# Kernel optimization log

Hardware: AMD Instinct MI355X
Metric: run time of the kernel (lower is better)

## Reference

```python
import jax, jax.numpy as jnp
import numpy as np

EMBED_DIM = 1024
NUM_HEADS = 16
HEAD_DIM = EMBED_DIM // NUM_HEADS
R_QKV = 256
R_OUT = 256
B, T = 4, 2048


def setup_inputs() -> dict:
    key = jax.random.key(0)
    k1, k2, k3, k4, k5 = jax.random.split(key, 5)
    s = 0.02
    return {
        "x": jax.random.normal(k1, (B, T, EMBED_DIM), dtype=jnp.float32),
        "W_qkv_v": jax.random.normal(k2, (R_QKV, EMBED_DIM), dtype=jnp.float32) * s,
        "W_qkv_u": jax.random.normal(k3, (3 * EMBED_DIM, R_QKV), dtype=jnp.float32) * s,
        "W_o_v": jax.random.normal(k4, (R_OUT, EMBED_DIM), dtype=jnp.float32) * s,
        "W_o_u": jax.random.normal(k5, (EMBED_DIM, R_OUT), dtype=jnp.float32) * s,
    }


def reference(x, W_qkv_v, W_qkv_u, W_o_v, W_o_u):
    Bq, Tq, C = x.shape
    H, D = NUM_HEADS, HEAD_DIM
    # low-rank qkv projection: x @ V^T @ U^T (torch Linear weight is [out,in])
    qkv = (x @ W_qkv_v.T) @ W_qkv_u.T  # [B,T,3C]
    q, k, v = jnp.split(qkv, 3, axis=-1)
    # split heads -> [B,H,T,D]
    q = q.reshape(Bq, Tq, H, D).transpose(0, 2, 1, 3)
    k = k.reshape(Bq, Tq, H, D).transpose(0, 2, 1, 3)
    v = v.reshape(Bq, Tq, H, D).transpose(0, 2, 1, 3)
    scale = 1.0 / jnp.sqrt(jnp.asarray(D, dtype=x.dtype))
    scores = jnp.einsum('bhtd,bhsd->bhts', q, k) * scale  # [B,H,T,T]
    # softmax in fp32 then cast back, matching torch.softmax(dtype=float32)
    attn = jax.nn.softmax(scores.astype(jnp.float32), axis=-1).astype(q.dtype)
    y = jnp.einsum('bhts,bhsd->bhtd', attn, v)  # [B,H,T,D]
    y = y.transpose(0, 2, 1, 3).reshape(Bq, Tq, C)  # merge heads
    # low-rank output projection
    y = (y @ W_o_v.T) @ W_o_u.T
    return y
```

## Files before the change

### kernel.cpp

```cpp
#include <hip/hip_runtime.h>
#include <hip/hip_bf16.h>

typedef __attribute__((ext_vector_type(8))) short short8;
typedef __attribute__((ext_vector_type(4))) float f32x4;
typedef __attribute__((ext_vector_type(16))) float f32x16;
typedef unsigned short u16;
typedef unsigned int u32;

__device__ __forceinline__ void gload_lds16(const void* g, void* l) {
  typedef const __attribute__((address_space(1))) u32 gu32;
  typedef __attribute__((address_space(3))) u32 lu32;
  __builtin_amdgcn_global_load_lds((gu32*)g, (lu32*)l, 16, 0, 0);
}

__device__ __forceinline__ u16 f2bf(float f) {
  union { float f; u32 u; } v; v.f = f;
  u32 u = v.u + 0x7FFFu + ((v.u >> 16) & 1u);
  return (u16)(u >> 16);
}

__device__ __forceinline__ u32 cvtpk(float lo, float hiv) {
  u32 r;
  asm("v_cvt_pk_bf16_f32 %0, %1, %2" : "=v"(r) : "v"(lo), "v"(hiv));
  return r;
}

__device__ __forceinline__ void plswap(u32& a, u32& b) {
  asm("v_permlane32_swap_b32 %0, %1" : "+v"(a), "+v"(b));
}

__device__ __forceinline__ float fexp2(float x) {
  float r;
  asm("v_exp_f32 %0, %1" : "=v"(r) : "v"(x));
  return r;
}

__device__ __forceinline__ short8 lds_read8(const u16* base, int byteoff) {
  return *(const short8*)((const char*)base + byteoff);
}

__global__ __launch_bounds__(256) void cast_w_kernel(
    const float* __restrict__ wv, const float* __restrict__ wu,
    const float* __restrict__ wov, const float* __restrict__ wou,
    u16* __restrict__ dst) {
  const long N0 = 262144, N1 = N0 + 786432, N2 = N1 + 262144, N3 = N2 + 262144;
  long i = (long)(blockIdx.x * 256 + threadIdx.x) * 8;
  if (i >= N3) return;
  const float* s;
  if (i < N0) s = wv + i;
  else if (i < N1) s = wu + (i - N0);
  else if (i < N2) s = wov + (i - N1);
  else s = wou + (i - N2);
  float4 a = *(const float4*)s;
  float4 b = *(const float4*)(s + 4);
  short8 o;
  o[0] = (short)f2bf(a.x); o[1] = (short)f2bf(a.y);
  o[2] = (short)f2bf(a.z); o[3] = (short)f2bf(a.w);
  o[4] = (short)f2bf(b.x); o[5] = (short)f2bf(b.y);
  o[6] = (short)f2bf(b.z); o[7] = (short)f2bf(b.w);
  *(short8*)(dst + i) = o;
}

template<int BM, int BN, int MR, int NR, typename OutT>
__global__ __launch_bounds__(256) void gemm_bt(
    OutT* __restrict__ C, const u16* __restrict__ A, const u16* __restrict__ B,
    int N, int K) {
  __shared__ u16 As[BM * 64];
  __shared__ u16 Bs[BN * 64];
  const int tid = threadIdx.x;
  const int l = tid & 63, w = tid >> 6;
  const int wr = w >> 1, wc = w & 1;
  const int bm = blockIdx.x * BM, bn = blockIdx.y * BN;
  const int srow = l >> 3, sslot = (l & 7) ^ srow;

  f32x4 acc[MR][NR] = {};

  const u16* Ag = A + (long)(bm + srow) * K + sslot * 8;
  const u16* Bg = B + (long)(bn + srow) * K + sslot * 8;
  constexpr int CA = BM / 32, CB = BN / 32;

  for (int kt = 0; kt < K; kt += 64) {
#pragma unroll
    for (int c = 0; c < CA; ++c) {
      int ch = w * CA + c;
      gload_lds16(Ag + (long)ch * 8 * K + kt, (char*)As + ch * 1024);
    }
#pragma unroll
    for (int c = 0; c < CB; ++c) {
      int ch = w * CB + c;
      gload_lds16(Bg + (long)ch * 8 * K + kt, (char*)Bs + ch * 1024);
    }
    __syncthreads();
    short8 af[MR][2], bf[NR][2];
#pragma unroll
    for (int i = 0; i < MR; ++i)
#pragma unroll
      for (int kk = 0; kk < 2; ++kk) {
        int row = wr * (MR * 16) + i * 16 + (l & 15);
        af[i][kk] = lds_read8(As, row * 128 + (((kk * 4 + (l >> 4)) ^ (l & 7)) * 16));
      }
#pragma unroll
    for (int j = 0; j < NR; ++j)
#pragma unroll
      for (int kk = 0; kk < 2; ++kk) {
        int col = wc * (NR * 16) + j * 16 + (l & 15);
        bf[j][kk] = lds_read8(Bs, col * 128 + (((kk * 4 + (l >> 4)) ^ (l & 7)) * 16));
      }
#pragma unroll
    for (int kk = 0; kk < 2; ++kk)
#pragma unroll
      for (int i = 0; i < MR; ++i)
#pragma unroll
        for (int j = 0; j < NR; ++j)
          acc[i][j] = __builtin_amdgcn_mfma_f32_16x16x32_bf16(
              af[i][kk], bf[j][kk], acc[i][j], 0, 0, 0);
    __syncthreads();
  }
#pragma unroll
  for (int i = 0; i < MR; ++i)
#pragma unroll
    for (int j = 0; j < NR; ++j) {
      int row = bm + wr * (MR * 16) + i * 16 + (l >> 4) * 4;
      int col = bn + wc * (NR * 16) + j * 16 + (l & 15);
#pragma unroll
      for (int r = 0; r < 4; ++r) {
        if constexpr (sizeof(OutT) == 4) {
          C[(long)(row + r) * N + col] = acc[i][j][r];
        } else {
          ((u16*)C)[(long)(row + r) * N + col] = f2bf(acc[i][j][r]);
        }
      }
    }
}

__global__ __launch_bounds__(256) void gemm_a32(
    u16* __restrict__ C, const float* __restrict__ A, const u16* __restrict__ B,
    int N, int K) {
  constexpr int BM = 64, BN = 64, MR = 2, NR = 2;
  __shared__ u16 As[BM * 64];
  __shared__ u16 Bs[BN * 64];
  const int tid = threadIdx.x;
  const int l = tid & 63, w = tid >> 6;
  const int wr = w >> 1, wc = w & 1;
  const int bm = blockIdx.x * BM, bn = blockIdx.y * BN;
  const int srow = l >> 3, sslot = (l & 7) ^ srow;

  f32x4 acc[MR][NR] = {};
  const u16* Bg = B + (long)(bn + srow) * K + sslot * 8;

  for (int kt = 0; kt < K; kt += 64) {
#pragma unroll
    for (int c = 0; c < 2; ++c) {
      int ch = w * 2 + c;
      gload_lds16(Bg + (long)ch * 8 * K + kt, (char*)Bs + ch * 1024);
    }
#pragma unroll
    for (int it = 0; it < 2; ++it) {
      int c = tid + it * 256;
      int row = c >> 3, slot = c & 7;
      const float* src = A + (long)(bm + row) * K + kt + slot * 8;
      float4 a = *(const float4*)src;
      float4 b = *(const float4*)(src + 4);
      union { u32 u[4]; short8 s; } pk;
      pk.u[0] = cvtpk(a.x, a.y);
      pk.u[1] = cvtpk(a.z, a.w);
      pk.u[2] = cvtpk(b.x, b.y);
      pk.u[3] = cvtpk(b.z, b.w);
      *(short8*)((char*)As + row * 128 + ((slot ^ (row & 7)) * 16)) = pk.s;
    }
    __syncthreads();
    short8 af[MR][2], bf[NR][2];
#pragma unroll
    for (int i = 0; i < MR; ++i)
#pragma unroll
      for (int kk = 0; kk < 2; ++kk) {
        int row = wr * (MR * 16) + i * 16 + (l & 15);
        af[i][kk] = lds_read8(As, row * 128 + (((kk * 4 + (l >> 4)) ^ (l & 7)) * 16));
      }
#pragma unroll
    for (int j = 0; j < NR; ++j)
#pragma unroll
      for (int kk = 0; kk < 2; ++kk) {
        int col = wc * (NR * 16) + j * 16 + (l & 15);
        bf[j][kk] = lds_read8(Bs, col * 128 + (((kk * 4 + (l >> 4)) ^ (l & 7)) * 16));
      }
#pragma unroll
    for (int kk = 0; kk < 2; ++kk)
#pragma unroll
      for (int i = 0; i < MR; ++i)
#pragma unroll
        for (int j = 0; j < NR; ++j)
          acc[i][j] = __builtin_amdgcn_mfma_f32_16x16x32_bf16(
              af[i][kk], bf[j][kk], acc[i][j], 0, 0, 0);
    __syncthreads();
  }
#pragma unroll
  for (int i = 0; i < MR; ++i)
#pragma unroll
    for (int j = 0; j < NR; ++j) {
      int row = bm + wr * (MR * 16) + i * 16 + (l >> 4) * 4;
      int col = bn + wc * (NR * 16) + j * 16 + (l & 15);
#pragma unroll
      for (int r = 0; r < 4; ++r)
        C[(long)(row + r) * N + col] = f2bf(acc[i][j][r]);
    }
}

__global__ __launch_bounds__(256) void vtrans_kernel(
    u16* __restrict__ Vt, const u16* __restrict__ QKV) {
  constexpr int T = 2048, LDQ = 3072;
  __shared__ u16 L[64 * 80];
  const int tid = threadIdx.x;
  const int t0 = blockIdx.x * 64, bh = blockIdx.y;
  const int b = bh >> 4, h = bh & 15;
  const u16* src = QKV + (long)b * T * LDQ + 2048 + h * 64;
#pragma unroll
  for (int it = 0; it < 2; ++it) {
    int row = (tid >> 3) + it * 32;
    int d0 = (tid & 7) * 8;
    short8 v = *(const short8*)(src + (long)(t0 + row) * LDQ + d0);
#pragma unroll
    for (int j = 0; j < 8; ++j)
      L[(d0 + j) * 80 + row] = (u16)(short)v[j];
  }
  __syncthreads();
  u16* dst = Vt + (long)bh * 64 * T + t0;
#pragma unroll
  for (int it = 0; it < 2; ++it) {
    int d = (tid >> 3) + it * 32;
    int c = (tid & 7) * 8;
    *(short8*)(dst + (long)d * T + c) = *(const short8*)(&L[d * 80 + c]);
  }
}

__global__ __launch_bounds__(512, 4) void attn_kernel(
    u16* __restrict__ Y, const u16* __restrict__ QKV, const u16* __restrict__ Vt) {
  constexpr int T = 2048, LDQ = 3072, NT = T / 64;
  constexpr float SC = 0.18033688011112042f;
  __shared__ u16 SMEM[24576];
  const int tid = threadIdx.x, l = tid & 63, w = tid >> 6;
  const int lq = l & 31, hi = l >> 5;
  const int bh = blockIdx.x, qt = blockIdx.y;
  const int b = bh >> 4, h = bh & 15;
  const long base = (long)b * T * LDQ;
  const int q0 = qt * 256 + w * 32;

  short8 qf[4];
#pragma unroll
  for (int ks = 0; ks < 4; ++ks)
    qf[ks] = *(const short8*)(QKV + base + (long)(q0 + lq) * LDQ + h * 64 +
                              ks * 16 + hi * 8);

  const short8 ONES = {(short)0x3F80, (short)0x3F80, (short)0x3F80, (short)0x3F80,
                       (short)0x3F80, (short)0x3F80, (short)0x3F80, (short)0x3F80};

  f32x16 o0 = {}, o1 = {}, olr = {};

  const int c = tid;
  const int kr = c >> 3, ds = (c & 7) ^ (kr & 7);
  const u16* Kg = QKV + base + 1024 + h * 64;
  const u16* Vg = Vt + (long)bh * 64 * T;

  auto STAGE = [&](int kt, int s) {
    u16* Kd = SMEM + s * 8192;
    u16* Vd = Kd + 4096;
    gload_lds16(Kg + (long)(kt + kr) * LDQ + ds * 8, (char*)Kd + c * 16);
    gload_lds16(Vg + (long)kr * T + kt + ds * 8, (char*)Vd + c * 16);
  };

  const int pslA[4] = {((0 + hi) ^ (lq & 7)) * 16, ((2 + hi) ^ (lq & 7)) * 16,
                       ((4 + hi) ^ (lq & 7)) * 16, ((6 + hi) ^ (lq & 7)) * 16};

  auto COMPUTE = [&](const u16* Ks, const u16* Vs) {
    f32x16 p0 = {}, p1 = {};
    __builtin_amdgcn_s_setprio(1);
#pragma unroll
    for (int ks = 0; ks < 4; ++ks) {
      short8 ka = lds_read8(Ks, lq * 128 + pslA[ks]);
      short8 kb = lds_read8(Ks, (32 + lq) * 128 + pslA[ks]);
      p0 = __builtin_amdgcn_mfma_f32_32x32x16_bf16(ka, qf[ks], p0, 0, 0, 0);
      p1 = __builtin_amdgcn_mfma_f32_32x32x16_bf16(kb, qf[ks], p1, 0, 0, 0);
    }
    __builtin_amdgcn_s_setprio(0);
    p0 = p0 * SC;
    p1 = p1 * SC;
#pragma unroll
    for (int r = 0; r < 16; ++r) p0[r] = fexp2(p0[r]);
#pragma unroll
    for (int r = 0; r < 16; ++r) p1[r] = fexp2(p1[r]);
    __builtin_amdgcn_s_setprio(1);
#pragma unroll
    for (int ks = 0; ks < 4; ++ks) {
      const f32x16& ps = (ks < 2) ? p0 : p1;
      const int r0 = (ks & 1) * 8;
      u32 uA = cvtpk(ps[r0 + 0], ps[r0 + 1]);
      u32 uB = cvtpk(ps[r0 + 2], ps[r0 + 3]);
      u32 uC = cvtpk(ps[r0 + 4], ps[r0 + 5]);
      u32 uD = cvtpk(ps[r0 + 6], ps[r0 + 7]);
      plswap(uA, uC);
      plswap(uB, uD);
      union { u32 u[4]; short8 s; } pb;
      pb.u[0] = uA; pb.u[1] = uB; pb.u[2] = uC; pb.u[3] = uD;
      short8 va = lds_read8(Vs, lq * 128 + pslA[ks]);
      short8 vb = lds_read8(Vs, (32 + lq) * 128 + pslA[ks]);
      o0 = __builtin_amdgcn_mfma_f32_32x32x16_bf16(va, pb.s, o0, 0, 0, 0);
      o1 = __builtin_amdgcn_mfma_f32_32x32x16_bf16(vb, pb.s, o1, 0, 0, 0);
      olr = __builtin_amdgcn_mfma_f32_32x32x16_bf16(ONES, pb.s, olr, 0, 0, 0);
    }
    __builtin_amdgcn_s_setprio(0);
  };

  STAGE(0, 0);
  STAGE(64, 1);
  for (int t = 0; t < NT; ++t) {
    if (t + 1 < NT) {
      asm volatile("s_waitcnt vmcnt(2)" ::: "memory");
    } else {
      asm volatile("s_waitcnt vmcnt(0)" ::: "memory");
    }
    __builtin_amdgcn_s_barrier();
    __builtin_amdgcn_sched_barrier(0);
    if (t + 2 < NT) STAGE((t + 2) * 64, (t + 2) % 3);
    const u16* Ks = SMEM + (t % 3) * 8192;
    COMPUTE(Ks, Ks + 4096);
  }

  __syncthreads();
  float inv = 1.0f / olr[0];
  const int row = w * 32 + lq;
#pragma unroll
  for (int df = 0; df < 2; ++df)
#pragma unroll
    for (int r = 0; r < 16; ++r) {
      int d = df * 32 + (r & 3) + 8 * (r >> 2) + 4 * hi;
      float v = (df ? o1[r] : o0[r]) * inv;
      *(u16*)((char*)SMEM + row * 128 + (((d >> 3) ^ (row & 7)) * 16) + (d & 7) * 2) =
          f2bf(v);
    }
  __syncthreads();
#pragma unroll
  for (int it = 0; it < 4; ++it) {
    int cc = tid + it * 512;
    int q = cc >> 3, g = cc & 7;
    int pg = g ^ (q & 7);
    short8 vv = *(const short8*)((const char*)SMEM + q * 128 + pg * 16);
    *(short8*)(Y + (long)(b * T + qt * 256 + q) * 1024 + h * 64 + g * 8) = vv;
  }
}

__global__ void ws_too_small_kernel(float* out) { out[0] = 3.0e38f; }

extern "C" void kernel_launch(void* const* d_in, const int* in_sizes, int n_in,
                              void* d_out, int out_size, void* d_ws, size_t ws_size,
                              hipStream_t stream) {
  (void)in_sizes; (void)n_in; (void)out_size;
  const float* x   = (const float*)d_in[0];
  const float* wv  = (const float*)d_in[1];
  const float* wu  = (const float*)d_in[2];
  const float* wov = (const float*)d_in[3];
  const float* wou = (const float*)d_in[4];
  float* out = (float*)d_out;
  u16* ws = (u16*)d_ws;

  u16* wvb  = ws;
  u16* wub  = ws + 262144;
  u16* wovb = ws + 1048576;
  u16* woub = ws + 1310720;
  u16* t    = ws + 1572864;
  u16* qkv  = ws + 3670016;
  u16* vt   = ws + 28835840;
  u16* yb   = ws + 37224448;
  u16* z    = ws + 45613056;

  if (ws_size < 95420416ull) {
    ws_too_small_kernel<<<1, 1, 0, stream>>>(out);
    return;
  }

  cast_w_kernel<<<dim3(768), dim3(256), 0, stream>>>(wv, wu, wov, wou, ws);
  gemm_a32<<<dim3(128, 4), dim3(256), 0, stream>>>(t, x, wvb, 256, 1024);
  gemm_bt<128, 128, 4, 4, u16><<<dim3(64, 24), dim3(256), 0, stream>>>(qkv, t, wub, 3072, 256);
  vtrans_kernel<<<dim3(32, 64), dim3(256), 0, stream>>>(vt, qkv);
  attn_kernel<<<dim3(64, 8), dim3(512), 0, stream>>>(yb, qkv, vt);
  gemm_bt<64, 64, 2, 2, u16><<<dim3(128, 4), dim3(256), 0, stream>>>(z, yb, wovb, 256, 1024);
  gemm_bt<128, 128, 4, 4, float><<<dim3(64, 8), dim3(256), 0, stream>>>(out, z, woub, 1024, 256);
}
```

Before: 168.5 us.

## Compute V transposed directly via batched GEMM, dropping the transpose kernel

The QKV projection now writes only Q and K (row stride 2048). V^T is produced per batch by a batched GEMM of W_u's V rows against t, writing the [h,d,t] layout attention expects. The separate vtrans kernel and its round trip through the V part of the qkv buffer go away. Attention now indexes Q/K with the narrower stride, and gemm_bt gains per-z batch strides.

```diff
diff --git a/kernel.cpp b/kernel.cpp
--- a/kernel.cpp
+++ b/kernel.cpp
@@ -64,13 +64,17 @@
 template<int BM, int BN, int MR, int NR, typename OutT>
 __global__ __launch_bounds__(256) void gemm_bt(
     OutT* __restrict__ C, const u16* __restrict__ A, const u16* __restrict__ B,
-    int N, int K) {
+    int N, int K, long sA, long sB, long sC) {
   __shared__ u16 As[BM * 64];
   __shared__ u16 Bs[BN * 64];
   const int tid = threadIdx.x;
   const int l = tid & 63, w = tid >> 6;
   const int wr = w >> 1, wc = w & 1;
   const int bm = blockIdx.x * BM, bn = blockIdx.y * BN;
+  const long bz = blockIdx.z;
+  A += bz * sA;
+  B += bz * sB;
+  C += bz * sC;
   const int srow = l >> 3, sslot = (l & 7) ^ srow;
 
   f32x4 acc[MR][NR] = {};
@@ -206,36 +210,9 @@
     }
 }
 
-__global__ __launch_bounds__(256) void vtrans_kernel(
-    u16* __restrict__ Vt, const u16* __restrict__ QKV) {
-  constexpr int T = 2048, LDQ = 3072;
-  __shared__ u16 L[64 * 80];
-  const int tid = threadIdx.x;
-  const int t0 = blockIdx.x * 64, bh = blockIdx.y;
-  const int b = bh >> 4, h = bh & 15;
-  const u16* src = QKV + (long)b * T * LDQ + 2048 + h * 64;
-#pragma unroll
-  for (int it = 0; it < 2; ++it) {
-    int row = (tid >> 3) + it * 32;
-    int d0 = (tid & 7) * 8;
-    short8 v = *(const short8*)(src + (long)(t0 + row) * LDQ + d0);
-#pragma unroll
-    for (int j = 0; j < 8; ++j)
-      L[(d0 + j) * 80 + row] = (u16)(short)v[j];
-  }
-  __syncthreads();
-  u16* dst = Vt + (long)bh * 64 * T + t0;
-#pragma unroll
-  for (int it = 0; it < 2; ++it) {
-    int d = (tid >> 3) + it * 32;
-    int c = (tid & 7) * 8;
-    *(short8*)(dst + (long)d * T + c) = *(const short8*)(&L[d * 80 + c]);
-  }
-}
-
 __global__ __launch_bounds__(512, 4) void attn_kernel(
     u16* __restrict__ Y, const u16* __restrict__ QKV, const u16* __restrict__ Vt) {
-  constexpr int T = 2048, LDQ = 3072, NT = T / 64;
+  constexpr int T = 2048, LDQ = 2048, NT = T / 64;
   constexpr float SC = 0.18033688011112042f;
   __shared__ u16 SMEM[24576];
   const int tid = threadIdx.x, l = tid & 63, w = tid >> 6;
@@ -367,7 +344,7 @@
   u16* wovb = ws + 1048576;
   u16* woub = ws + 1310720;
   u16* t    = ws + 1572864;
-  u16* qkv  = ws + 3670016;
+  u16* qk   = ws + 3670016;
   u16* vt   = ws + 28835840;
   u16* yb   = ws + 37224448;
   u16* z    = ws + 45613056;
@@ -379,9 +356,13 @@
 
   cast_w_kernel<<<dim3(768), dim3(256), 0, stream>>>(wv, wu, wov, wou, ws);
   gemm_a32<<<dim3(128, 4), dim3(256), 0, stream>>>(t, x, wvb, 256, 1024);
-  gemm_bt<128, 128, 4, 4, u16><<<dim3(64, 24), dim3(256), 0, stream>>>(qkv, t, wub, 3072, 256);
-  vtrans_kernel<<<dim3(32, 64), dim3(256), 0, stream>>>(vt, qkv);
-  attn_kernel<<<dim3(64, 8), dim3(512), 0, stream>>>(yb, qkv, vt);
-  gemm_bt<64, 64, 2, 2, u16><<<dim3(128, 4), dim3(256), 0, stream>>>(z, yb, wovb, 256, 1024);
-  gemm_bt<128, 128, 4, 4, float><<<dim3(64, 8), dim3(256), 0, stream>>>(out, z, woub, 1024, 256);
-}
+  gemm_bt<128, 128, 4, 4, u16><<<dim3(64, 16), dim3(256), 0, stream>>>(
+      qk, t, wub, 2048, 256, 0, 0, 0);
+  gemm_bt<64, 64, 2, 2, u16><<<dim3(16, 32, 4), dim3(256), 0, stream>>>(
+      vt, wub + 2048 * 256, t, 2048, 256, 0, 2048 * 256, 1024 * 2048);
+  attn_kernel<<<dim3(64, 8), dim3(512), 0, stream>>>(yb, qk, vt);
+  gemm_bt<64, 64, 2, 2, u16><<<dim3(128, 4), dim3(256), 0, stream>>>(
+      z, yb, wovb, 256, 1024, 0, 0, 0);
+  gemm_bt<128, 128, 4, 4, float><<<dim3(64, 8), dim3(256), 0, stream>>>(
+      out, z, woub, 1024, 256, 0, 0, 0);
+}
```

Measured after the change: 172.1 us. 1.02x slower.
